# Optimization experiments

Measured on AMD Instinct MI355X. Metric: run time of the kernel, lower is better.

Reference implementation:

```python
import jax, jax.numpy as jnp
import numpy as np

B, T, E, H = 2, 2048, 2048, 16
D = E // H


def setup_inputs() -> dict:
    key = jax.random.key(0)
    ks = jax.random.split(key, 5)
    s = 0.02
    return {
        "x": jax.random.normal(ks[0], (B, T, E), jnp.float32),
        "Wq": jax.random.normal(ks[1], (E, E), jnp.float32) * s,
        "Wk": jax.random.normal(ks[2], (E, E), jnp.float32) * s,
        "Wv": jax.random.normal(ks[3], (E, E), jnp.float32) * s,
        "Wp": jax.random.normal(ks[4], (E, E), jnp.float32) * s,
        "bp": jnp.zeros((E,), jnp.float32),
    }


def reference(x, Wq, Wk, Wv, Wp, bp):
    b, t, e = x.shape
    h, d = H, E // H
    # torch Linear: y = x @ W.T (no bias for qkv)
    Q = (x @ Wq.T).reshape(b, h, t, d)  # faithful: view without transpose
    K = (x @ Wk.T).reshape(b, h, t, d)
    V = (x @ Wv.T).reshape(b, h, t, d)
    scores = jnp.einsum("bhqd,bhkd->bhqk", Q, K)
    causal = jnp.triu(jnp.ones((t, t), bool), k=1)  # True above diagonal
    scores = jnp.where(causal, -jnp.inf, scores)
    weights = jax.nn.softmax(scores / jnp.sqrt(jnp.float32(d)), axis=-1)
    # dropout p=0.0 (eval) -> identity
    ctx = jnp.einsum("bhqk,bhkd->bhqd", weights, V)  # (b,h,t,d)
    ctx = ctx.transpose(0, 2, 1, 3).reshape(b, t, e)
    return ctx @ Wp.T + bp
```

## Files before the change

### kernel.cpp

```cpp
#include <hip/hip_runtime.h>

#define SEQ   2048
#define EMB   2048
#define NHEAD 16
#define HDIM  128
#define ROWSM 4096

typedef float  f32x4   __attribute__((ext_vector_type(4)));
typedef float  f32x16  __attribute__((ext_vector_type(16)));
typedef __bf16 bf16x8  __attribute__((ext_vector_type(8)));

__device__ __forceinline__ unsigned short f2bf(float f) {
  union { __bf16 b; unsigned short u; } v; v.b = (__bf16)f; return v.u;
}
__device__ __forceinline__ unsigned int pk2(float a, float b) {
  return (unsigned int)f2bf(a) | ((unsigned int)f2bf(b) << 16);
}
__device__ __forceinline__ float max3f(float a, float b, float c) {
  return fmaxf(fmaxf(a, b), c);
}

__device__ __forceinline__ void gload16(const void* g, void* l) {
  __builtin_amdgcn_global_load_lds(
      (__attribute__((address_space(1))) const unsigned int*)g,
      (__attribute__((address_space(3))) unsigned int*)l,
      16, 0, 0);
}

__global__ void cvt_all(const float* __restrict__ x,  const float* __restrict__ Wq,
                        const float* __restrict__ Wk, const float* __restrict__ Wv,
                        const float* __restrict__ Wp, unsigned short* __restrict__ xb,
                        unsigned short* __restrict__ WB3, unsigned short* __restrict__ Wb,
                        int nX4, int nW4) {
  const int z = blockIdx.z;
  const float* in;
  unsigned short* out;
  int n4;
  if (z == 0)      { in = x;  out = xb;  n4 = nX4; }
  else if (z == 1) { in = Wq; out = WB3;                          n4 = nW4; }
  else if (z == 2) { in = Wk; out = WB3 + (size_t)EMB * EMB;      n4 = nW4; }
  else if (z == 3) { in = Wv; out = WB3 + (size_t)2 * EMB * EMB;  n4 = nW4; }
  else             { in = Wp; out = Wb;  n4 = nW4; }
  int i = blockIdx.x * 256 + threadIdx.x;
  if (i >= n4) return;
  float4 v = ((const float4*)in)[i];
  ushort4 o4;
  o4.x = f2bf(v.x); o4.y = f2bf(v.y); o4.z = f2bf(v.z); o4.w = f2bf(v.w);
  ((ushort4*)out)[i] = o4;
}

__global__ __launch_bounds__(512, 1) void gemm192_qkv(
    const unsigned short* __restrict__ A, const unsigned short* __restrict__ B,
    unsigned short* __restrict__ Cb) {
  __shared__ __align__(16) unsigned short At[2][256 * 64];
  __shared__ __align__(16) unsigned short Bt[2][192 * 64];

  const int tid  = threadIdx.x;
  const int lane = tid & 63;
  const int w    = tid >> 6;
  const int wr   = w >> 2;
  const int wc   = w & 3;
  const int lg   = lane >> 4;
  const int lc   = lane & 15;

  const int bid = blockIdx.x;
  const int xcd = bid & 7;
  const int j   = bid >> 3;
  const int mt  = xcd * 2 + (j >> 5);
  const int nt  = j & 31;
  const int m0 = mt * 256;
  const int n0 = nt * 192;

  const int srow8 = lane >> 3;
  const int sslot = (lane & 7) ^ srow8;
  const int NT = EMB / 64;

  auto stageAeven = [&](int ts) {
    if (ts >= NT) return;
    int buf = ts & 1, k0 = ts * 64;
    { int c = w;      int row = c * 8 + srow8;
      gload16(A + (size_t)(m0 + row) * EMB + k0 + sslot * 8, (char*)&At[buf][0] + c * 1024); }
    { int c = 16 + w; int row = c * 8 + srow8;
      gload16(A + (size_t)(m0 + row) * EMB + k0 + sslot * 8, (char*)&At[buf][0] + c * 1024); }
  };
  auto stageAodd = [&](int ts) {
    if (ts >= NT) return;
    int buf = ts & 1, k0 = ts * 64;
    { int c = 8 + w;  int row = c * 8 + srow8;
      gload16(A + (size_t)(m0 + row) * EMB + k0 + sslot * 8, (char*)&At[buf][0] + c * 1024); }
    { int c = 24 + w; int row = c * 8 + srow8;
      gload16(A + (size_t)(m0 + row) * EMB + k0 + sslot * 8, (char*)&At[buf][0] + c * 1024); }
  };
  auto stageB = [&](int ts) {
    if (ts >= NT) return;
    int buf = ts & 1, k0 = ts * 64;
#pragma unroll
    for (int s = 0; s < 3; ++s) {
      int c = w + s * 8;
      int row = c * 8 + srow8;
      gload16(B + (size_t)(n0 + row) * EMB + k0 + sslot * 8, (char*)&Bt[buf][0] + c * 1024);
    }
  };

  f32x4 acc[8][3] = {};
  bf16x8 afr[4][2], bfr[3][2];

  stageAeven(0); stageB(0); stageAodd(0); stageAeven(1); stageB(1);
  asm volatile("s_waitcnt vmcnt(7)" ::: "memory");
  __builtin_amdgcn_s_barrier();

  for (int t = 0; t < NT; ++t) {
    const char* ab = (const char*)&At[t & 1][0];
    const char* bb = (const char*)&Bt[t & 1][0];

#pragma unroll
    for (int ni = 0; ni < 3; ++ni)
#pragma unroll
      for (int kk = 0; kk < 2; ++kk) {
        int row = wc * 48 + ni * 16 + lc;
        bfr[ni][kk] = *(const bf16x8*)(bb + row * 128 + ((((kk << 2) | lg) ^ (lc & 7)) << 4));
      }
#pragma unroll
    for (int mi = 0; mi < 4; ++mi)
#pragma unroll
      for (int kk = 0; kk < 2; ++kk) {
        int row = wr * 128 + mi * 16 + lc;
        afr[mi][kk] = *(const bf16x8*)(ab + row * 128 + ((((kk << 2) | lg) ^ (lc & 7)) << 4));
      }
    stageAodd(t + 1);
    __builtin_amdgcn_s_barrier();
    asm volatile("s_waitcnt lgkmcnt(0)" ::: "memory");
    __builtin_amdgcn_sched_barrier(0);
    __builtin_amdgcn_s_setprio(1);
#pragma unroll
    for (int mi = 0; mi < 4; ++mi)
#pragma unroll
      for (int ni = 0; ni < 3; ++ni)
#pragma unroll
        for (int kk = 0; kk < 2; ++kk)
          acc[mi][ni] = __builtin_amdgcn_mfma_f32_16x16x32_bf16(
              afr[mi][kk], bfr[ni][kk], acc[mi][ni], 0, 0, 0);
    __builtin_amdgcn_s_setprio(0);
    if (t + 1 < NT) asm volatile("s_waitcnt vmcnt(7)" ::: "memory");
    else            asm volatile("s_waitcnt vmcnt(0)" ::: "memory");
    __builtin_amdgcn_s_barrier();

#pragma unroll
    for (int mi = 0; mi < 4; ++mi)
#pragma unroll
      for (int kk = 0; kk < 2; ++kk) {
        int row = wr * 128 + 64 + mi * 16 + lc;
        afr[mi][kk] = *(const bf16x8*)(ab + row * 128 + ((((kk << 2) | lg) ^ (lc & 7)) << 4));
      }
    stageAeven(t + 2); stageB(t + 2);
    __builtin_amdgcn_s_barrier();
    asm volatile("s_waitcnt lgkmcnt(0)" ::: "memory");
    __builtin_amdgcn_sched_barrier(0);
    __builtin_amdgcn_s_setprio(1);
#pragma unroll
    for (int mi = 0; mi < 4; ++mi)
#pragma unroll
      for (int ni = 0; ni < 3; ++ni)
#pragma unroll
        for (int kk = 0; kk < 2; ++kk)
          acc[4 + mi][ni] = __builtin_amdgcn_mfma_f32_16x16x32_bf16(
              afr[mi][kk], bfr[ni][kk], acc[4 + mi][ni], 0, 0, 0);
    __builtin_amdgcn_s_setprio(0);
    if (t + 2 < NT)      asm volatile("s_waitcnt vmcnt(7)" ::: "memory");
    else if (t + 1 < NT) asm volatile("s_waitcnt vmcnt(2)" ::: "memory");
    __builtin_amdgcn_s_barrier();
  }

#pragma unroll
  for (int mi = 0; mi < 8; ++mi)
#pragma unroll
    for (int ni = 0; ni < 3; ++ni) {
      int col = n0 + wc * 48 + ni * 16 + lc;
      unsigned short* dst = Cb + (size_t)(col >> 11) * ROWSM * EMB + (col & 2047);
#pragma unroll
      for (int rr = 0; rr < 4; ++rr) {
        int row = m0 + wr * 128 + mi * 16 + lg * 4 + rr;
        dst[(size_t)row * EMB] = f2bf(acc[mi][ni][rr]);
      }
    }
}

__global__ __launch_bounds__(512, 1) void gemm_p8(
    const unsigned short* __restrict__ A, const unsigned short* __restrict__ B,
    float* __restrict__ Cout, const float* __restrict__ bias) {
  __shared__ __align__(16) unsigned short At[2][128 * 64];
  __shared__ __align__(16) unsigned short Bt[2][256 * 64];

  const int tid  = threadIdx.x;
  const int lane = tid & 63;
  const int w    = tid >> 6;
  const int wr   = w >> 2;
  const int wc   = w & 3;
  const int lg   = lane >> 4;
  const int lc   = lane & 15;

  const int bid = blockIdx.x;
  const int xcd = bid & 7;
  const int j   = bid >> 3;
  const int mt  = xcd * 4 + (j >> 3);
  const int nt  = j & 7;
  const int m0 = mt * 128;
  const int n0 = nt * 256;

  const int srow8 = lane >> 3;
  const int sslot = (lane & 7) ^ srow8;
  const int NT = EMB / 64;

  auto stageA = [&](int ts) {
    if (ts >= NT) return;
    int buf = ts & 1, k0 = ts * 64;
#pragma unroll
    for (int rr = 0; rr < 2; ++rr) {
      int c = w + rr * 8;
      int row = c * 8 + srow8;
      gload16(A + (size_t)(m0 + row) * EMB + k0 + sslot * 8, (char*)&At[buf][0] + c * 1024);
    }
  };
  auto stageBlow = [&](int ts) {
    if (ts >= NT) return;
    int buf = ts & 1, k0 = ts * 64;
#pragma unroll
    for (int rr = 0; rr < 2; ++rr) {
      int i = w + rr * 8;
      int c = (i >> 2) * 8 + (i & 3);
      int row = c * 8 + srow8;
      gload16(B + (size_t)(n0 + row) * EMB + k0 + sslot * 8, (char*)&Bt[buf][0] + c * 1024);
    }
  };
  auto stageBhigh = [&](int ts) {
    if (ts >= NT) return;
    int buf = ts & 1, k0 = ts * 64;
#pragma unroll
    for (int rr = 0; rr < 2; ++rr) {
      int i = w + rr * 8;
      int c = (i >> 2) * 8 + 4 + (i & 3);
      int row = c * 8 + srow8;
      gload16(B + (size_t)(n0 + row) * EMB + k0 + sslot * 8, (char*)&Bt[buf][0] + c * 1024);
    }
  };

  f32x4 acc[4][4] = {};
  bf16x8 afr[4][2], bfr0[2][2], bfr1[2][2];

  stageA(0); stageBlow(0); stageBhigh(0); stageA(1); stageBlow(1);
  asm volatile("s_waitcnt vmcnt(6)" ::: "memory");
  __builtin_amdgcn_s_barrier();

  for (int t = 0; t < NT; ++t) {
    const char* ab = (const char*)&At[t & 1][0];
    const char* bb = (const char*)&Bt[t & 1][0];

#pragma unroll
    for (int ni = 0; ni < 2; ++ni)
#pragma unroll
      for (int kk = 0; kk < 2; ++kk) {
        int row = wc * 64 + ni * 16 + lc;
        bfr0[ni][kk] = *(const bf16x8*)(bb + row * 128 + ((((kk << 2) | lg) ^ (lc & 7)) << 4));
      }
#pragma unroll
    for (int mi = 0; mi < 4; ++mi)
#pragma unroll
      for (int kk = 0; kk < 2; ++kk) {
        int row = wr * 64 + mi * 16 + lc;
        afr[mi][kk] = *(const bf16x8*)(ab + row * 128 + ((((kk << 2) | lg) ^ (lc & 7)) << 4));
      }
    stageBhigh(t + 1);
    __builtin_amdgcn_s_barrier();
    asm volatile("s_waitcnt lgkmcnt(0)" ::: "memory");
    __builtin_amdgcn_sched_barrier(0);
    __builtin_amdgcn_s_setprio(1);
#pragma unroll
    for (int mi = 0; mi < 4; ++mi)
#pragma unroll
      for (int ni = 0; ni < 2; ++ni)
#pragma unroll
        for (int kk = 0; kk < 2; ++kk)
          acc[mi][ni] = __builtin_amdgcn_mfma_f32_16x16x32_bf16(
              afr[mi][kk], bfr0[ni][kk], acc[mi][ni], 0, 0, 0);
    __builtin_amdgcn_s_setprio(0);
    if (t + 1 < NT) asm volatile("s_waitcnt vmcnt(6)" ::: "memory");
    else            asm volatile("s_waitcnt vmcnt(0)" ::: "memory");
    __builtin_amdgcn_s_barrier();

#pragma unroll
    for (int ni = 0; ni < 2; ++ni)
#pragma unroll
      for (int kk = 0; kk < 2; ++kk) {
        int row = wc * 64 + 32 + ni * 16 + lc;
        bfr1[ni][kk] = *(const bf16x8*)(bb + row * 128 + ((((kk << 2) | lg) ^ (lc & 7)) << 4));
      }
    stageA(t + 2); stageBlow(t + 2);
    __builtin_amdgcn_s_barrier();
    asm volatile("s_waitcnt lgkmcnt(0)" ::: "memory");
    __builtin_amdgcn_sched_barrier(0);
    __builtin_amdgcn_s_setprio(1);
#pragma unroll
    for (int mi = 0; mi < 4; ++mi)
#pragma unroll
      for (int ni = 0; ni < 2; ++ni)
#pragma unroll
        for (int kk = 0; kk < 2; ++kk)
          acc[mi][2 + ni] = __builtin_amdgcn_mfma_f32_16x16x32_bf16(
              afr[mi][kk], bfr1[ni][kk], acc[mi][2 + ni], 0, 0, 0);
    __builtin_amdgcn_s_setprio(0);
    if (t + 2 < NT)      asm volatile("s_waitcnt vmcnt(6)" ::: "memory");
    else if (t + 1 < NT) asm volatile("s_waitcnt vmcnt(2)" ::: "memory");
    __builtin_amdgcn_s_barrier();
  }

#pragma unroll
  for (int mi = 0; mi < 4; ++mi)
#pragma unroll
    for (int ni = 0; ni < 4; ++ni) {
      int col = n0 + wc * 64 + ((ni >> 1) * 32) + (ni & 1) * 16 + lc;
#pragma unroll
      for (int rr = 0; rr < 4; ++rr) {
        int row = m0 + wr * 64 + mi * 16 + lg * 4 + rr;
        Cout[(size_t)row * EMB + col] = acc[mi][ni][rr] + bias[col];
      }
    }
}

__global__ __launch_bounds__(256, 2) void attn_causal(
    const unsigned short* __restrict__ Pq, const unsigned short* __restrict__ Pk,
    const unsigned short* __restrict__ Pv, unsigned short* __restrict__ ctx) {
  __shared__ __align__(16) unsigned short Ks[2][64 * 128];
  __shared__ __align__(16) unsigned short Vt[2][128 * 64];

  const int tid  = threadIdx.x;
  const int lane = tid & 63;
  const int w    = tid >> 6;
  const int ql   = lane & 31;
  const int hi   = lane >> 5;
  const int lg   = lane >> 4;
  const int lc   = lane & 15;

  const int bid = blockIdx.x;
  const int xcd = bid & 7;
  const int jj_ = bid >> 3;
  const int hh  = jj_ >> 4;
  const int bh  = xcd * 4 + hh;
  const int b   = bh >> 4;
  const int h   = bh & 15;
  const int qtr = jj_ & 15;
  const int qt  = (hh >= 2) ? (15 - qtr) : qtr;
  const int q0 = qt * 128;
  const int qw = q0 + w * 32;
  const int qg = qw + ql;

  const size_t hoff = (size_t)bh * SEQ * HDIM;
  const unsigned short* Q  = Pq + hoff;
  const unsigned short* Kh = Pk + hoff;
  const unsigned short* Vh = Pv + hoff;

  bf16x8 bq[8];
#pragma unroll
  for (int d8 = 0; d8 < 8; ++d8)
    bq[d8] = *(const bf16x8*)(Q + (size_t)qg * HDIM + d8 * 16 + hi * 8);

  const float NEG = -3.0e38f;
  f32x16 o[4];
#pragma unroll
  for (int dt = 0; dt < 4; ++dt)
#pragma unroll
    for (int r = 0; r < 16; ++r) o[dt][r] = 0.f;
  float m_r = NEG, l_r = 0.f;

  const float Cs   = 0.12753123161692858f;
  const float TDEF = 62.7f;

  auto stageK = [&](int buf, int t) {
    int kv0 = t * 64;
#pragma unroll
    for (int ii = 0; ii < 4; ++ii) {
      int i = w * 4 + ii;
      int r = i * 4 + lg;
      int sd = lc ^ (r & 7);
      gload16(Kh + (size_t)(kv0 + r) * HDIM + sd * 8, (char*)&Ks[buf][0] + i * 1024);
    }
  };
  auto loadV = [&](uint4* vr, int t) {
    int kv0 = t * 64;
#pragma unroll
    for (int uu = 0; uu < 2; ++uu) {
      int u = tid + uu * 256;
      int kp = u >> 4, dg = u & 15;
      int k = kp * 2, d0 = dg * 8;
      vr[uu * 2]     = *(const uint4*)(Vh + (size_t)(kv0 + k) * HDIM + d0);
      vr[uu * 2 + 1] = *(const uint4*)(Vh + (size_t)(kv0 + k + 1) * HDIM + d0);
    }
  };
  auto packV = [&](int buf, const uint4* vr) {
#pragma unroll
    for (int uu = 0; uu < 2; ++uu) {
      int u = tid + uu * 256;
      int kp = u >> 4, dg = u & 15;
      int k = kp * 2, d0 = dg * 8;
      const unsigned short* e0 = (const unsigned short*)&vr[uu * 2];
      const unsigned short* e1 = (const unsigned short*)&vr[uu * 2 + 1];
#pragma unroll
      for (int jj = 0; jj < 8; ++jj) {
        int d = d0 + jj;
        int slot = (k >> 3) ^ jj ^ (dg & 7);
        int byteoff = d * 128 + (slot << 4) + (k & 7) * 2;
        *(unsigned int*)((char*)&Vt[buf][0] + byteoff) =
            (unsigned int)e0[jj] | ((unsigned int)e1[jj] << 16);
      }
    }
  };

  const int ntiles = 2 * qt + 2;
  uint4 vr[4];

  loadV(vr, 0); stageK(0, 0);
  asm volatile("s_waitcnt vmcnt(4)" ::: "memory");
  packV(0, vr);
  loadV(vr, 1); stageK(1, 1);
  asm volatile("s_waitcnt vmcnt(8)" ::: "memory");
  asm volatile("s_waitcnt lgkmcnt(0)" ::: "memory");
  __builtin_amdgcn_s_barrier();

  for (int t = 0; t < ntiles; ++t) {
    const int buf = t & 1;
    const bool hasN1 = (t + 1 < ntiles);
    const bool hasN2 = (t + 2 < ntiles);
    const int kv0 = t * 64;

    if (hasN1) {
      asm volatile("s_waitcnt vmcnt(4)" ::: "memory");
      packV(buf ^ 1, vr);
      if (hasN2) loadV(vr, t + 2);
    }

    if (kv0 <= qw + 31) {
      const bool s1on = (kv0 + 32 <= qw + 31);
      const bool diag = (kv0 + 63 > qw);
      const char* ksb = (const char*)&Ks[buf][0];
      const char* vtb = (const char*)&Vt[buf][0];

      f32x16 c0, c1;
#pragma unroll
      for (int r = 0; r < 16; ++r) { c0[r] = 0.f; c1[r] = s1on ? 0.f : NEG; }
      __builtin_amdgcn_s_setprio(1);
#pragma unroll
      for (int d8 = 0; d8 < 8; ++d8) {
        bf16x8 ak = *(const bf16x8*)(ksb + ql * 256 +
                                     (((d8 * 2 + hi) ^ (ql & 7)) << 4));
        c0 = __builtin_amdgcn_mfma_f32_32x32x16_bf16(ak, bq[d8], c0, 0, 0, 0);
      }
      if (s1on) {
#pragma unroll
        for (int d8 = 0; d8 < 8; ++d8) {
          bf16x8 ak = *(const bf16x8*)(ksb + (32 + ql) * 256 +
                                       (((d8 * 2 + hi) ^ (ql & 7)) << 4));
          c1 = __builtin_amdgcn_mfma_f32_32x32x16_bf16(ak, bq[d8], c1, 0, 0, 0);
        }
      }
      __builtin_amdgcn_s_setprio(0);

      if (diag) {
#pragma unroll
        for (int r = 0; r < 16; ++r) {
          int kvl = (r & 3) + 8 * (r >> 2) + 4 * hi;
          if (kv0 + kvl > qg) c0[r] = NEG;
          if (s1on && kv0 + 32 + kvl > qg) c1[r] = NEG;
        }
      }
      float rm;
      {
        float a0 = max3f(c0[0],  c0[1],  c0[2]);
        float a1 = max3f(c0[3],  c0[4],  c0[5]);
        float a2 = max3f(c0[6],  c0[7],  c0[8]);
        float a3 = max3f(c0[9],  c0[10], c0[11]);
        float a4 = max3f(c0[12], c0[13], c0[14]);
        float a5 = max3f(c0[15], c1[0],  c1[1]);
        float a6 = max3f(c1[2],  c1[3],  c1[4]);
        float a7 = max3f(c1[5],  c1[6],  c1[7]);
        float a8 = max3f(c1[8],  c1[9],  c1[10]);
        float a9 = max3f(c1[11], c1[12], c1[13]);
        float aa = fmaxf(c1[14], c1[15]);
        float b0 = max3f(a0, a1, a2);
        float b1 = max3f(a3, a4, a5);
        float b2 = max3f(a6, a7, a8);
        float b3 = max3f(a9, aa, NEG);
        rm = fmaxf(fmaxf(b0, b1), fmaxf(b2, b3));
      }
      rm = fmaxf(rm, __shfl_xor(rm, 32));

      if (__any(rm > m_r + TDEF)) {
        float mnew = fmaxf(m_r, rm);
        float alpha = exp2f((m_r - mnew) * Cs);
        m_r = mnew;
        l_r *= alpha;
#pragma unroll
        for (int r = 0; r < 16; ++r) {
          float ar = __shfl(alpha, (r & 3) + 8 * (r >> 2) + 4 * hi);
#pragma unroll
          for (int dt = 0; dt < 4; ++dt) o[dt][r] *= ar;
        }
      }
#pragma unroll
      for (int r = 0; r < 16; ++r) {
        c0[r] = exp2f((c0[r] - m_r) * Cs);
        c1[r] = exp2f((c1[r] - m_r) * Cs);
      }
      float ps = 0.f;
#pragma unroll
      for (int r = 0; r < 16; ++r) ps += c0[r] + c1[r];
      ps += __shfl_xor(ps, 32);
      l_r += ps;

      bf16x8 pa[4];
#pragma unroll
      for (int t4 = 0; t4 < 4; ++t4) {
        const f32x16& cc = (t4 < 2) ? c0 : c1;
        const int rA = (t4 & 1) * 8;
        unsigned int pkL0 = pk2(cc[rA + 0], cc[rA + 1]);
        unsigned int pkL1 = pk2(cc[rA + 2], cc[rA + 3]);
        unsigned int pkH0 = pk2(cc[rA + 4], cc[rA + 5]);
        unsigned int pkH1 = pk2(cc[rA + 6], cc[rA + 7]);
        unsigned int give0 = hi ? pkL0 : pkH0;
        unsigned int give1 = hi ? pkL1 : pkH1;
        unsigned int keep0 = hi ? pkH0 : pkL0;
        unsigned int keep1 = hi ? pkH1 : pkL1;
        unsigned int recv0 = __shfl_xor(give0, 32);
        unsigned int recv1 = __shfl_xor(give1, 32);
        union { unsigned int u[4]; bf16x8 v; } pu;
        pu.u[0] = hi ? recv0 : keep0;
        pu.u[1] = hi ? recv1 : keep1;
        pu.u[2] = hi ? keep0 : recv0;
        pu.u[3] = hi ? keep1 : recv1;
        pa[t4] = pu.v;
      }
      __builtin_amdgcn_s_setprio(1);
#pragma unroll
      for (int t4 = 0; t4 < 4; ++t4) {
        if (diag && kv0 + t4 * 16 > qw + 31) continue;
#pragma unroll
        for (int dt = 0; dt < 4; ++dt) {
          int d = dt * 32 + ql;
          int slot = ((t4 << 1) | hi) ^ (d & 7) ^ ((d >> 3) & 7);
          bf16x8 bv = *(const bf16x8*)(vtb + d * 128 + (slot << 4));
          o[dt] = __builtin_amdgcn_mfma_f32_32x32x16_bf16(pa[t4], bv, o[dt], 0, 0, 0);
        }
      }
      __builtin_amdgcn_s_setprio(0);
    }

    if (hasN2) stageK(buf, t + 2);
    asm volatile("s_waitcnt lgkmcnt(0)" ::: "memory");
    if (hasN1) {
      if (hasN2) asm volatile("s_waitcnt vmcnt(8)" ::: "memory");
      else       asm volatile("s_waitcnt vmcnt(0)" ::: "memory");
    }
    __builtin_amdgcn_s_barrier();
  }

  float linv = 1.0f / l_r;
  unsigned short* outp = ctx + (size_t)b * SEQ * EMB + (size_t)h * HDIM;
#pragma unroll
  for (int r = 0; r < 16; ++r) {
    int kvl = (r & 3) + 8 * (r >> 2) + 4 * hi;
    float lr = __shfl(linv, kvl);
    int qrow = qw + kvl;
#pragma unroll
    for (int dt = 0; dt < 4; ++dt)
      outp[(size_t)qrow * EMB + dt * 32 + ql] = f2bf(o[dt][r] * lr);
  }
}

extern "C" void kernel_launch(void* const* d_in, const int* in_sizes, int n_in,
                              void* d_out, int out_size, void* d_ws, size_t ws_size,
                              hipStream_t stream) {
  const float* x  = (const float*)d_in[0];
  const float* Wq = (const float*)d_in[1];
  const float* Wk = (const float*)d_in[2];
  const float* Wv = (const float*)d_in[3];
  const float* Wp = (const float*)d_in[4];
  const float* bp = (const float*)d_in[5];

  char* ws = (char*)d_ws;
  unsigned short* xb = (unsigned short*)ws;
  unsigned short* Wb = (unsigned short*)(ws + (size_t)(16u << 20));
  unsigned short* Pq = (unsigned short*)(ws + (size_t)(24u << 20));
  unsigned short* Pk = (unsigned short*)(ws + (size_t)(40u << 20));
  unsigned short* Pv = (unsigned short*)(ws + (size_t)(56u << 20));
  unsigned short* WB3 = (unsigned short*)d_out;

  const int nX4 = ROWSM * EMB / 4;
  const int nW4 = EMB * EMB / 4;

  cvt_all<<<dim3(nX4 / 256, 1, 5), 256, 0, stream>>>(
      x, Wq, Wk, Wv, Wp, xb, WB3, Wb, nX4, nW4);

  gemm192_qkv<<<512, 512, 0, stream>>>(xb, WB3, Pq);

  attn_causal<<<512, 256, 0, stream>>>(Pq, Pk, Pv, xb);

  gemm_p8<<<256, 512, 0, stream>>>(xb, Wb, (float*)d_out, bp);
}
```

Measured before the change: 257.0 us.

## Shrink attention blocks to 64-query tiles and drop double-buffered K/V pipeline

The attention kernel now runs 1024 blocks of 128 threads, each covering 64 query rows instead of 128, with the block-to-head/tile mapping reworked to match. The double-buffered K/V staging with prefetch and manual vmcnt waits is replaced by a single LDS buffer loaded synchronously each iteration between two __syncthreads. This cuts LDS use and allows more resident blocks for better occupancy and finer causal load balance. In exchange, global loads no longer overlap with compute, and each K/V tile is reloaded by twice as many blocks.

```diff
diff --git a/kernel.cpp b/kernel.cpp
--- a/kernel.cpp
+++ b/kernel.cpp
@@ -326,11 +326,11 @@
     }
 }
 
-__global__ __launch_bounds__(256, 2) void attn_causal(
+__global__ __launch_bounds__(128, 2) void attn_causal(
     const unsigned short* __restrict__ Pq, const unsigned short* __restrict__ Pk,
     const unsigned short* __restrict__ Pv, unsigned short* __restrict__ ctx) {
-  __shared__ __align__(16) unsigned short Ks[2][64 * 128];
-  __shared__ __align__(16) unsigned short Vt[2][128 * 64];
+  __shared__ __align__(16) unsigned short Ks[64 * 128];
+  __shared__ __align__(16) unsigned short Vt[128 * 64];
 
   const int tid  = threadIdx.x;
   const int lane = tid & 63;
@@ -342,14 +342,14 @@
 
   const int bid = blockIdx.x;
   const int xcd = bid & 7;
-  const int jj_ = bid >> 3;
-  const int hh  = jj_ >> 4;
+  const int j   = bid >> 3;
+  const int hh  = j >> 5;
   const int bh  = xcd * 4 + hh;
   const int b   = bh >> 4;
   const int h   = bh & 15;
-  const int qtr = jj_ & 15;
-  const int qt  = (hh >= 2) ? (15 - qtr) : qtr;
-  const int q0 = qt * 128;
+  const int qtr = j & 31;
+  const int qt  = (hh & 1) ? (31 - qtr) : qtr;
+  const int q0 = qt * 64;
   const int qw = q0 + w * 32;
   const int qg = qw + ql;
 
@@ -374,191 +374,149 @@
   const float Cs   = 0.12753123161692858f;
   const float TDEF = 62.7f;
 
-  auto stageK = [&](int buf, int t) {
-    int kv0 = t * 64;
-#pragma unroll
-    for (int ii = 0; ii < 4; ++ii) {
-      int i = w * 4 + ii;
+  const int ntiles = qt + 1;
+  for (int t = 0; t < ntiles; ++t) {
+    const int kv0 = t * 64;
+    if (t) __syncthreads();
+#pragma unroll
+    for (int ii = 0; ii < 8; ++ii) {
+      int i = w * 8 + ii;
       int r = i * 4 + lg;
       int sd = lc ^ (r & 7);
-      gload16(Kh + (size_t)(kv0 + r) * HDIM + sd * 8, (char*)&Ks[buf][0] + i * 1024);
-    }
-  };
-  auto loadV = [&](uint4* vr, int t) {
-    int kv0 = t * 64;
-#pragma unroll
-    for (int uu = 0; uu < 2; ++uu) {
-      int u = tid + uu * 256;
+      gload16(Kh + (size_t)(kv0 + r) * HDIM + sd * 8, (char*)Ks + i * 1024);
+    }
+#pragma unroll
+    for (int uu = 0; uu < 4; ++uu) {
+      int u = tid + uu * 128;
       int kp = u >> 4, dg = u & 15;
       int k = kp * 2, d0 = dg * 8;
-      vr[uu * 2]     = *(const uint4*)(Vh + (size_t)(kv0 + k) * HDIM + d0);
-      vr[uu * 2 + 1] = *(const uint4*)(Vh + (size_t)(kv0 + k + 1) * HDIM + d0);
-    }
-  };
-  auto packV = [&](int buf, const uint4* vr) {
-#pragma unroll
-    for (int uu = 0; uu < 2; ++uu) {
-      int u = tid + uu * 256;
-      int kp = u >> 4, dg = u & 15;
-      int k = kp * 2, d0 = dg * 8;
-      const unsigned short* e0 = (const unsigned short*)&vr[uu * 2];
-      const unsigned short* e1 = (const unsigned short*)&vr[uu * 2 + 1];
+      uint4 r0 = *(const uint4*)(Vh + (size_t)(kv0 + k) * HDIM + d0);
+      uint4 r1 = *(const uint4*)(Vh + (size_t)(kv0 + k + 1) * HDIM + d0);
+      const unsigned short* e0 = (const unsigned short*)&r0;
+      const unsigned short* e1 = (const unsigned short*)&r1;
 #pragma unroll
       for (int jj = 0; jj < 8; ++jj) {
         int d = d0 + jj;
         int slot = (k >> 3) ^ jj ^ (dg & 7);
         int byteoff = d * 128 + (slot << 4) + (k & 7) * 2;
-        *(unsigned int*)((char*)&Vt[buf][0] + byteoff) =
+        *(unsigned int*)((char*)Vt + byteoff) =
             (unsigned int)e0[jj] | ((unsigned int)e1[jj] << 16);
       }
     }
-  };
-
-  const int ntiles = 2 * qt + 2;
-  uint4 vr[4];
-
-  loadV(vr, 0); stageK(0, 0);
-  asm volatile("s_waitcnt vmcnt(4)" ::: "memory");
-  packV(0, vr);
-  loadV(vr, 1); stageK(1, 1);
-  asm volatile("s_waitcnt vmcnt(8)" ::: "memory");
-  asm volatile("s_waitcnt lgkmcnt(0)" ::: "memory");
-  __builtin_amdgcn_s_barrier();
-
-  for (int t = 0; t < ntiles; ++t) {
-    const int buf = t & 1;
-    const bool hasN1 = (t + 1 < ntiles);
-    const bool hasN2 = (t + 2 < ntiles);
-    const int kv0 = t * 64;
-
-    if (hasN1) {
-      asm volatile("s_waitcnt vmcnt(4)" ::: "memory");
-      packV(buf ^ 1, vr);
-      if (hasN2) loadV(vr, t + 2);
-    }
-
-    if (kv0 <= qw + 31) {
-      const bool s1on = (kv0 + 32 <= qw + 31);
-      const bool diag = (kv0 + 63 > qw);
-      const char* ksb = (const char*)&Ks[buf][0];
-      const char* vtb = (const char*)&Vt[buf][0];
-
-      f32x16 c0, c1;
-#pragma unroll
-      for (int r = 0; r < 16; ++r) { c0[r] = 0.f; c1[r] = s1on ? 0.f : NEG; }
-      __builtin_amdgcn_s_setprio(1);
+    __syncthreads();
+
+    const bool s1on = (kv0 + 32 <= qw + 31);
+    const bool diag = (kv0 + 63 > qw);
+    const char* ksb = (const char*)Ks;
+    const char* vtb = (const char*)Vt;
+
+    f32x16 c0, c1;
+#pragma unroll
+    for (int r = 0; r < 16; ++r) { c0[r] = 0.f; c1[r] = s1on ? 0.f : NEG; }
+    __builtin_amdgcn_s_setprio(1);
+#pragma unroll
+    for (int d8 = 0; d8 < 8; ++d8) {
+      bf16x8 ak = *(const bf16x8*)(ksb + ql * 256 +
+                                   (((d8 * 2 + hi) ^ (ql & 7)) << 4));
+      c0 = __builtin_amdgcn_mfma_f32_32x32x16_bf16(ak, bq[d8], c0, 0, 0, 0);
+    }
+    if (s1on) {
 #pragma unroll
       for (int d8 = 0; d8 < 8; ++d8) {
-        bf16x8 ak = *(const bf16x8*)(ksb + ql * 256 +
+        bf16x8 ak = *(const bf16x8*)(ksb + (32 + ql) * 256 +
                                      (((d8 * 2 + hi) ^ (ql & 7)) << 4));
-        c0 = __builtin_amdgcn_mfma_f32_32x32x16_bf16(ak, bq[d8], c0, 0, 0, 0);
-      }
-      if (s1on) {
-#pragma unroll
-        for (int d8 = 0; d8 < 8; ++d8) {
-          bf16x8 ak = *(const bf16x8*)(ksb + (32 + ql) * 256 +
-                                       (((d8 * 2 + hi) ^ (ql & 7)) << 4));
-          c1 = __builtin_amdgcn_mfma_f32_32x32x16_bf16(ak, bq[d8], c1, 0, 0, 0);
-        }
-      }
-      __builtin_amdgcn_s_setprio(0);
-
-      if (diag) {
-#pragma unroll
-        for (int r = 0; r < 16; ++r) {
-          int kvl = (r & 3) + 8 * (r >> 2) + 4 * hi;
-          if (kv0 + kvl > qg) c0[r] = NEG;
-          if (s1on && kv0 + 32 + kvl > qg) c1[r] = NEG;
-        }
-      }
-      float rm;
-      {
-        float a0 = max3f(c0[0],  c0[1],  c0[2]);
-        float a1 = max3f(c0[3],  c0[4],  c0[5]);
-        float a2 = max3f(c0[6],  c0[7],  c0[8]);
-        float a3 = max3f(c0[9],  c0[10], c0[11]);
-        float a4 = max3f(c0[12], c0[13], c0[14]);
-        float a5 = max3f(c0[15], c1[0],  c1[1]);
-        float a6 = max3f(c1[2],  c1[3],  c1[4]);
-        float a7 = max3f(c1[5],  c1[6],  c1[7]);
-        float a8 = max3f(c1[8],  c1[9],  c1[10]);
-        float a9 = max3f(c1[11], c1[12], c1[13]);
-        float aa = fmaxf(c1[14], c1[15]);
-        float b0 = max3f(a0, a1, a2);
-        float b1 = max3f(a3, a4, a5);
-        float b2 = max3f(a6, a7, a8);
-        float b3 = max3f(a9, aa, NEG);
-        rm = fmaxf(fmaxf(b0, b1), fmaxf(b2, b3));
-      }
-      rm = fmaxf(rm, __shfl_xor(rm, 32));
-
-      if (__any(rm > m_r + TDEF)) {
-        float mnew = fmaxf(m_r, rm);
-        float alpha = exp2f((m_r - mnew) * Cs);
-        m_r = mnew;
-        l_r *= alpha;
-#pragma unroll
-        for (int r = 0; r < 16; ++r) {
-          float ar = __shfl(alpha, (r & 3) + 8 * (r >> 2) + 4 * hi);
-#pragma unroll
-          for (int dt = 0; dt < 4; ++dt) o[dt][r] *= ar;
-        }
-      }
+        c1 = __builtin_amdgcn_mfma_f32_32x32x16_bf16(ak, bq[d8], c1, 0, 0, 0);
+      }
+    }
+    __builtin_amdgcn_s_setprio(0);
+
+    if (diag) {
 #pragma unroll
       for (int r = 0; r < 16; ++r) {
-        c0[r] = exp2f((c0[r] - m_r) * Cs);
-        c1[r] = exp2f((c1[r] - m_r) * Cs);
-      }
-      float ps = 0.f;
-#pragma unroll
-      for (int r = 0; r < 16; ++r) ps += c0[r] + c1[r];
-      ps += __shfl_xor(ps, 32);
-      l_r += ps;
-
-      bf16x8 pa[4];
-#pragma unroll
-      for (int t4 = 0; t4 < 4; ++t4) {
-        const f32x16& cc = (t4 < 2) ? c0 : c1;
-        const int rA = (t4 & 1) * 8;
-        unsigned int pkL0 = pk2(cc[rA + 0], cc[rA + 1]);
-        unsigned int pkL1 = pk2(cc[rA + 2], cc[rA + 3]);
-        unsigned int pkH0 = pk2(cc[rA + 4], cc[rA + 5]);
-        unsigned int pkH1 = pk2(cc[rA + 6], cc[rA + 7]);
-        unsigned int give0 = hi ? pkL0 : pkH0;
-        unsigned int give1 = hi ? pkL1 : pkH1;
-        unsigned int keep0 = hi ? pkH0 : pkL0;
-        unsigned int keep1 = hi ? pkH1 : pkL1;
-        unsigned int recv0 = __shfl_xor(give0, 32);
-        unsigned int recv1 = __shfl_xor(give1, 32);
-        union { unsigned int u[4]; bf16x8 v; } pu;
-        pu.u[0] = hi ? recv0 : keep0;
-        pu.u[1] = hi ? recv1 : keep1;
-        pu.u[2] = hi ? keep0 : recv0;
-        pu.u[3] = hi ? keep1 : recv1;
-        pa[t4] = pu.v;
-      }
-      __builtin_amdgcn_s_setprio(1);
-#pragma unroll
-      for (int t4 = 0; t4 < 4; ++t4) {
-        if (diag && kv0 + t4 * 16 > qw + 31) continue;
-#pragma unroll
-        for (int dt = 0; dt < 4; ++dt) {
-          int d = dt * 32 + ql;
-          int slot = ((t4 << 1) | hi) ^ (d & 7) ^ ((d >> 3) & 7);
-          bf16x8 bv = *(const bf16x8*)(vtb + d * 128 + (slot << 4));
-          o[dt] = __builtin_amdgcn_mfma_f32_32x32x16_bf16(pa[t4], bv, o[dt], 0, 0, 0);
-        }
-      }
-      __builtin_amdgcn_s_setprio(0);
-    }
-
-    if (hasN2) stageK(buf, t + 2);
-    asm volatile("s_waitcnt lgkmcnt(0)" ::: "memory");
-    if (hasN1) {
-      if (hasN2) asm volatile("s_waitcnt vmcnt(8)" ::: "memory");
-      else       asm volatile("s_waitcnt vmcnt(0)" ::: "memory");
-    }
-    __builtin_amdgcn_s_barrier();
+        int kvl = (r & 3) + 8 * (r >> 2) + 4 * hi;
+        if (kv0 + kvl > qg) c0[r] = NEG;
+        if (s1on && kv0 + 32 + kvl > qg) c1[r] = NEG;
+      }
+    }
+    float rm;
+    {
+      float a0 = max3f(c0[0],  c0[1],  c0[2]);
+      float a1 = max3f(c0[3],  c0[4],  c0[5]);
+      float a2 = max3f(c0[6],  c0[7],  c0[8]);
+      float a3 = max3f(c0[9],  c0[10], c0[11]);
+      float a4 = max3f(c0[12], c0[13], c0[14]);
+      float a5 = max3f(c0[15], c1[0],  c1[1]);
+      float a6 = max3f(c1[2],  c1[3],  c1[4]);
+      float a7 = max3f(c1[5],  c1[6],  c1[7]);
+      float a8 = max3f(c1[8],  c1[9],  c1[10]);
+      float a9 = max3f(c1[11], c1[12], c1[13]);
+      float aa = fmaxf(c1[14], c1[15]);
+      float b0 = max3f(a0, a1, a2);
+      float b1 = max3f(a3, a4, a5);
+      float b2 = max3f(a6, a7, a8);
+      float b3 = max3f(a9, aa, NEG);
+      rm = fmaxf(fmaxf(b0, b1), fmaxf(b2, b3));
+    }
+    rm = fmaxf(rm, __shfl_xor(rm, 32));
+
+    if (__any(rm > m_r + TDEF)) {
+      float mnew = fmaxf(m_r, rm);
+      float alpha = exp2f((m_r - mnew) * Cs);
+      m_r = mnew;
+      l_r *= alpha;
+#pragma unroll
+      for (int r = 0; r < 16; ++r) {
+        float ar = __shfl(alpha, (r & 3) + 8 * (r >> 2) + 4 * hi);
+#pragma unroll
+        for (int dt = 0; dt < 4; ++dt) o[dt][r] *= ar;
+      }
+    }
+#pragma unroll
+    for (int r = 0; r < 16; ++r) {
+      c0[r] = exp2f((c0[r] - m_r) * Cs);
+      c1[r] = exp2f((c1[r] - m_r) * Cs);
+    }
+    float ps = 0.f;
+#pragma unroll
+    for (int r = 0; r < 16; ++r) ps += c0[r] + c1[r];
+    ps += __shfl_xor(ps, 32);
+    l_r += ps;
+
+    bf16x8 pa[4];
+#pragma unroll
+    for (int t4 = 0; t4 < 4; ++t4) {
+      const f32x16& cc = (t4 < 2) ? c0 : c1;
+      const int rA = (t4 & 1) * 8;
+      unsigned int pkL0 = pk2(cc[rA + 0], cc[rA + 1]);
+      unsigned int pkL1 = pk2(cc[rA + 2], cc[rA + 3]);
+      unsigned int pkH0 = pk2(cc[rA + 4], cc[rA + 5]);
+      unsigned int pkH1 = pk2(cc[rA + 6], cc[rA + 7]);
+      unsigned int give0 = hi ? pkL0 : pkH0;
+      unsigned int give1 = hi ? pkL1 : pkH1;
+      unsigned int keep0 = hi ? pkH0 : pkL0;
+      unsigned int keep1 = hi ? pkH1 : pkL1;
+      unsigned int recv0 = __shfl_xor(give0, 32);
+      unsigned int recv1 = __shfl_xor(give1, 32);
+      union { unsigned int u[4]; bf16x8 v; } pu;
+      pu.u[0] = hi ? recv0 : keep0;
+      pu.u[1] = hi ? recv1 : keep1;
+      pu.u[2] = hi ? keep0 : recv0;
+      pu.u[3] = hi ? keep1 : recv1;
+      pa[t4] = pu.v;
+    }
+    __builtin_amdgcn_s_setprio(1);
+#pragma unroll
+    for (int t4 = 0; t4 < 4; ++t4) {
+      if (diag && kv0 + t4 * 16 > qw + 31) continue;
+#pragma unroll
+      for (int dt = 0; dt < 4; ++dt) {
+        int d = dt * 32 + ql;
+        int slot = ((t4 << 1) | hi) ^ (d & 7) ^ ((d >> 3) & 7);
+        bf16x8 bv = *(const bf16x8*)(vtb + d * 128 + (slot << 4));
+        o[dt] = __builtin_amdgcn_mfma_f32_32x32x16_bf16(pa[t4], bv, o[dt], 0, 0, 0);
+      }
+    }
+    __builtin_amdgcn_s_setprio(0);
   }
 
   float linv = 1.0f / l_r;
@@ -600,7 +558,7 @@
 
   gemm192_qkv<<<512, 512, 0, stream>>>(xb, WB3, Pq);
 
-  attn_causal<<<512, 256, 0, stream>>>(Pq, Pk, Pv, xb);
+  attn_causal<<<1024, 128, 0, stream>>>(Pq, Pk, Pv, xb);
 
   gemm_p8<<<256, 512, 0, stream>>>(xb, Wb, (float*)d_out, bp);
 }
```

Result: slower. 267.9 us (+4.2%).

## Switch QKV GEMM to 32x32x16 MFMA with a 4x2 wave layout

Applied to the files above, without the earlier changes.

Changes the QKV projection GEMM from 16x16x32 bf16 MFMA tiles on a 2x4 wave grid to 32x32x16 MFMA tiles on a 4x2 wave grid. Each wave now covers 64 rows by 96 columns, and the LDS fragment reads, A-tile staging order and epilogue row mapping are rewritten to match. The larger MFMA shape should cut LDS fragment traffic per FLOP and the instruction count. In exchange, the wider tiles change register pressure and the LDS bank-conflict pattern under the existing XOR swizzle.

```diff
diff --git a/kernel.cpp b/kernel.cpp
--- a/kernel.cpp
+++ b/kernel.cpp
@@ -58,10 +58,10 @@
   const int tid  = threadIdx.x;
   const int lane = tid & 63;
   const int w    = tid >> 6;
-  const int wr   = w >> 2;
-  const int wc   = w & 3;
-  const int lg   = lane >> 4;
-  const int lc   = lane & 15;
+  const int wr   = w >> 1;
+  const int wc   = w & 1;
+  const int l31  = lane & 31;
+  const int l5   = lane >> 5;
 
   const int bid = blockIdx.x;
   const int xcd = bid & 7;
@@ -78,17 +78,17 @@
   auto stageAeven = [&](int ts) {
     if (ts >= NT) return;
     int buf = ts & 1, k0 = ts * 64;
-    { int c = w;      int row = c * 8 + srow8;
+    { int c = (w >> 2) * 8 + (w & 3);      int row = c * 8 + srow8;
       gload16(A + (size_t)(m0 + row) * EMB + k0 + sslot * 8, (char*)&At[buf][0] + c * 1024); }
-    { int c = 16 + w; int row = c * 8 + srow8;
+    { int c = (w >> 2) * 8 + (w & 3) + 16; int row = c * 8 + srow8;
       gload16(A + (size_t)(m0 + row) * EMB + k0 + sslot * 8, (char*)&At[buf][0] + c * 1024); }
   };
   auto stageAodd = [&](int ts) {
     if (ts >= NT) return;
     int buf = ts & 1, k0 = ts * 64;
-    { int c = 8 + w;  int row = c * 8 + srow8;
+    { int c = (w >> 2) * 8 + (w & 3) + 4;  int row = c * 8 + srow8;
       gload16(A + (size_t)(m0 + row) * EMB + k0 + sslot * 8, (char*)&At[buf][0] + c * 1024); }
-    { int c = 24 + w; int row = c * 8 + srow8;
+    { int c = (w >> 2) * 8 + (w & 3) + 20; int row = c * 8 + srow8;
       gload16(A + (size_t)(m0 + row) * EMB + k0 + sslot * 8, (char*)&At[buf][0] + c * 1024); }
   };
   auto stageB = [&](int ts) {
@@ -102,8 +102,8 @@
     }
   };
 
-  f32x4 acc[8][3] = {};
-  bf16x8 afr[4][2], bfr[3][2];
+  f32x16 acc[2][3] = {};
+  bf16x8 afr[4], bfr[3][4];
 
   stageAeven(0); stageB(0); stageAodd(0); stageAeven(1); stageB(1);
   asm volatile("s_waitcnt vmcnt(7)" ::: "memory");
@@ -114,57 +114,49 @@
     const char* bb = (const char*)&Bt[t & 1][0];
 
 #pragma unroll
-    for (int ni = 0; ni < 3; ++ni)
-#pragma unroll
-      for (int kk = 0; kk < 2; ++kk) {
-        int row = wc * 48 + ni * 16 + lc;
-        bfr[ni][kk] = *(const bf16x8*)(bb + row * 128 + ((((kk << 2) | lg) ^ (lc & 7)) << 4));
-      }
-#pragma unroll
-    for (int mi = 0; mi < 4; ++mi)
-#pragma unroll
-      for (int kk = 0; kk < 2; ++kk) {
-        int row = wr * 128 + mi * 16 + lc;
-        afr[mi][kk] = *(const bf16x8*)(ab + row * 128 + ((((kk << 2) | lg) ^ (lc & 7)) << 4));
-      }
+    for (int nf = 0; nf < 3; ++nf)
+#pragma unroll
+      for (int kk = 0; kk < 4; ++kk) {
+        int row = wc * 96 + nf * 32 + l31;
+        bfr[nf][kk] = *(const bf16x8*)(bb + row * 128 + ((((kk << 1) | l5) ^ (row & 7)) << 4));
+      }
+#pragma unroll
+    for (int kk = 0; kk < 4; ++kk) {
+      int row = wr * 64 + l31;
+      afr[kk] = *(const bf16x8*)(ab + row * 128 + ((((kk << 1) | l5) ^ (row & 7)) << 4));
+    }
     stageAodd(t + 1);
     __builtin_amdgcn_s_barrier();
     asm volatile("s_waitcnt lgkmcnt(0)" ::: "memory");
     __builtin_amdgcn_sched_barrier(0);
     __builtin_amdgcn_s_setprio(1);
 #pragma unroll
-    for (int mi = 0; mi < 4; ++mi)
-#pragma unroll
-      for (int ni = 0; ni < 3; ++ni)
-#pragma unroll
-        for (int kk = 0; kk < 2; ++kk)
-          acc[mi][ni] = __builtin_amdgcn_mfma_f32_16x16x32_bf16(
-              afr[mi][kk], bfr[ni][kk], acc[mi][ni], 0, 0, 0);
+    for (int nf = 0; nf < 3; ++nf)
+#pragma unroll
+      for (int kk = 0; kk < 4; ++kk)
+        acc[0][nf] = __builtin_amdgcn_mfma_f32_32x32x16_bf16(
+            afr[kk], bfr[nf][kk], acc[0][nf], 0, 0, 0);
     __builtin_amdgcn_s_setprio(0);
     if (t + 1 < NT) asm volatile("s_waitcnt vmcnt(7)" ::: "memory");
     else            asm volatile("s_waitcnt vmcnt(0)" ::: "memory");
     __builtin_amdgcn_s_barrier();
 
 #pragma unroll
-    for (int mi = 0; mi < 4; ++mi)
-#pragma unroll
-      for (int kk = 0; kk < 2; ++kk) {
-        int row = wr * 128 + 64 + mi * 16 + lc;
-        afr[mi][kk] = *(const bf16x8*)(ab + row * 128 + ((((kk << 2) | lg) ^ (lc & 7)) << 4));
-      }
+    for (int kk = 0; kk < 4; ++kk) {
+      int row = wr * 64 + 32 + l31;
+      afr[kk] = *(const bf16x8*)(ab + row * 128 + ((((kk << 1) | l5) ^ (row & 7)) << 4));
+    }
     stageAeven(t + 2); stageB(t + 2);
     __builtin_amdgcn_s_barrier();
     asm volatile("s_waitcnt lgkmcnt(0)" ::: "memory");
     __builtin_amdgcn_sched_barrier(0);
     __builtin_amdgcn_s_setprio(1);
 #pragma unroll
-    for (int mi = 0; mi < 4; ++mi)
-#pragma unroll
-      for (int ni = 0; ni < 3; ++ni)
-#pragma unroll
-        for (int kk = 0; kk < 2; ++kk)
-          acc[4 + mi][ni] = __builtin_amdgcn_mfma_f32_16x16x32_bf16(
-              afr[mi][kk], bfr[ni][kk], acc[4 + mi][ni], 0, 0, 0);
+    for (int nf = 0; nf < 3; ++nf)
+#pragma unroll
+      for (int kk = 0; kk < 4; ++kk)
+        acc[1][nf] = __builtin_amdgcn_mfma_f32_32x32x16_bf16(
+            afr[kk], bfr[nf][kk], acc[1][nf], 0, 0, 0);
     __builtin_amdgcn_s_setprio(0);
     if (t + 2 < NT)      asm volatile("s_waitcnt vmcnt(7)" ::: "memory");
     else if (t + 1 < NT) asm volatile("s_waitcnt vmcnt(2)" ::: "memory");
@@ -172,15 +164,15 @@
   }
 
 #pragma unroll
-  for (int mi = 0; mi < 8; ++mi)
-#pragma unroll
-    for (int ni = 0; ni < 3; ++ni) {
-      int col = n0 + wc * 48 + ni * 16 + lc;
+  for (int mf = 0; mf < 2; ++mf)
+#pragma unroll
+    for (int nf = 0; nf < 3; ++nf) {
+      int col = n0 + wc * 96 + nf * 32 + l31;
       unsigned short* dst = Cb + (size_t)(col >> 11) * ROWSM * EMB + (col & 2047);
 #pragma unroll
-      for (int rr = 0; rr < 4; ++rr) {
-        int row = m0 + wr * 128 + mi * 16 + lg * 4 + rr;
-        dst[(size_t)row * EMB] = f2bf(acc[mi][ni][rr]);
+      for (int r = 0; r < 16; ++r) {
+        int row = m0 + wr * 64 + mf * 32 + (r & 3) + 8 * (r >> 2) + 4 * l5;
+        dst[(size_t)row * EMB] = f2bf(acc[mf][nf][r]);
       }
     }
 }
```

Result: slower. 266.3 us (+3.6%).
